# Kernel tuning notes

Hardware: AMD Instinct MI355X
Metric: run time of the kernel (lower is better)

The kernel has to match this reference:

```python
import jax, jax.numpy as jnp
import numpy as np

TEMPERATURE = 0.5

def setup_inputs() -> dict:
    key = jax.random.key(0)
    k1, k2 = jax.random.split(key)
    N, D = 4096, 256
    z1 = jax.random.normal(k1, (N, D), dtype=jnp.float32)
    z2 = jax.random.normal(k2, (N, D), dtype=jnp.float32)
    return {"z1": z1, "z2": z2}

def reference(z1, z2):
    N, D = z1.shape
    # Interleave rows: Z[::2] = z1, Z[1::2] = z2  -> shape (2N, D)
    Z = jnp.stack([z1, z2], axis=1).reshape(2 * N, D).astype(jnp.float32)
    # L2 normalize rows (torch F.normalize default eps=1e-12)
    Z = Z / jnp.maximum(jnp.linalg.norm(Z, axis=1, keepdims=True), 1e-12)
    # Dense exp-similarity matrix (2N, 2N)
    S = jnp.exp(jnp.matmul(Z, Z.T) / TEMPERATURE)
    idx = jnp.arange(2 * N)
    diag = jnp.diagonal(S)
    rowsum = jnp.sum(S, axis=1)
    # positive pair of row i is row i^1 (2i <-> 2i+1)
    pos = S[idx, idx ^ 1]
    loss_per_row = -jnp.log(pos / (rowsum - diag + 1e-8))
    return jnp.sum(loss_per_row) / (2 * N)
```

## Files before the change

### kernel.cpp

```cpp
#include <hip/hip_runtime.h>
#include <hip/hip_bf16.h>
#include <stdint.h>

#define N2 8192
#define D 256
#define DB 512
#define RB_ROWS 256
#define WAVE_ROWS 64
#define CHUNK 32
#define JSPLIT 16
#define COLS_PER_BLOCK (N2 / JSPLIT)
#define CHUNKS_PER_BLOCK (COLS_PER_BLOCK / CHUNK)

using short8 = __attribute__((ext_vector_type(8))) short;
using f32x4  = __attribute__((ext_vector_type(4))) float;

__device__ inline unsigned short f2bf(float x) {
    union { float f; uint32_t u; } a; a.f = x;
    uint32_t r = (a.u + 0x7fff + ((a.u >> 16) & 1)) >> 16;
    return (unsigned short)r;
}

__global__ void knorm(const float* __restrict__ z1, const float* __restrict__ z2,
                      unsigned short* __restrict__ Zb, float* __restrict__ den) {
    int tid  = threadIdx.x;
    int lane = tid & 63;
    int w    = tid >> 6;
    int row  = blockIdx.x * 4 + w;
    const float* src = (row & 1) ? z2 : z1;
    int srow = row >> 1;
    float4 v = reinterpret_cast<const float4*>(src + (size_t)srow * D)[lane];
    float ss = v.x*v.x + v.y*v.y + v.z*v.z + v.w*v.w;
    #pragma unroll
    for (int off = 1; off < 64; off <<= 1) ss += __shfl_xor(ss, off);
    float inv = rsqrtf(ss);
    ushort4 o;
    o.x = f2bf(v.x * inv); o.y = f2bf(v.y * inv);
    o.z = f2bf(v.z * inv); o.w = f2bf(v.w * inv);
    *reinterpret_cast<ushort4*>(Zb + (size_t)row * D + lane * 4) = o;

    int gid = blockIdx.x * blockDim.x + tid;
    if (gid < N2) den[gid] = 0.f;
}

__launch_bounds__(256, 2)
__global__ void kmain(const unsigned short* __restrict__ Zb,
                      float* __restrict__ den, float* __restrict__ pos) {
    __shared__ char tile[CHUNK * DB];
    int tid  = threadIdx.x;
    int lane = tid & 63;
    int w    = tid >> 6;
    int bid  = blockIdx.x;
    int rb   = bid & 31;
    int js   = bid >> 5;
    int Rw   = rb * RB_ROWS + w * WAVE_ROWS;
    int Cbase = js * COLS_PER_BLOCK;
    int l15 = lane & 15, g = lane >> 4;

    const char* Zc = reinterpret_cast<const char*>(Zb);

    short8 A[4][8];
    #pragma unroll
    for (int mf = 0; mf < 4; ++mf) {
        const char* rowp = Zc + (size_t)(Rw + mf*16 + l15) * DB + g*16;
        #pragma unroll
        for (int s = 0; s < 8; ++s)
            A[mf][s] = *reinterpret_cast<const short8*>(rowp + s*64);
    }

    f32x4 acc[4][2];
    float rsum[4][4];
    #pragma unroll
    for (int mf = 0; mf < 4; ++mf) {
        #pragma unroll
        for (int r = 0; r < 4; ++r) rsum[mf][r] = 0.f;
        #pragma unroll
        for (int nf = 0; nf < 2; ++nf) acc[mf][nf] = (f32x4){0.f,0.f,0.f,0.f};
    }

    for (int c = 0; c < CHUNKS_PER_BLOCK; ++c) {
        int C0 = Cbase + c * CHUNK;
        __syncthreads();
        #pragma unroll
        for (int i = 0; i < 4; ++i) {
            int q  = tid + 256 * i;
            int r  = q >> 5;
            int cb = (q & 31) * 16;
            uint4 v = *reinterpret_cast<const uint4*>(Zc + (size_t)(C0 + r) * DB + cb);
            *reinterpret_cast<uint4*>(&tile[r * DB + (cb ^ ((r & 7) << 4))]) = v;
        }
        __syncthreads();

        #pragma unroll
        for (int s = 0; s < 8; ++s) {
            int cb = s*64 + g*16;
            int r0 = l15, r1 = 16 + l15;
            short8 B0 = *reinterpret_cast<const short8*>(&tile[r0 * DB + (cb ^ ((r0 & 7) << 4))]);
            short8 B1 = *reinterpret_cast<const short8*>(&tile[r1 * DB + (cb ^ ((r1 & 7) << 4))]);
            #pragma unroll
            for (int mf = 0; mf < 4; ++mf) {
                acc[mf][0] = __builtin_amdgcn_mfma_f32_16x16x32_bf16(A[mf][s], B0, acc[mf][0], 0, 0, 0);
                acc[mf][1] = __builtin_amdgcn_mfma_f32_16x16x32_bf16(A[mf][s], B1, acc[mf][1], 0, 0, 0);
            }
        }

        #pragma unroll
        for (int mf = 0; mf < 4; ++mf) {
            int Rt = Rw + mf * 16;
            #pragma unroll
            for (int nf = 0; nf < 2; ++nf) {
                int Ct = C0 + nf * 16;
                bool dg = (Ct == Rt);
                #pragma unroll
                for (int r = 0; r < 4; ++r) {
                    float v = acc[mf][nf][r];
                    float e = __expf(v + v);
                    if (dg) {
                        int rl = g * 4 + r;
                        if (l15 == rl) e = 0.f;
                        if (l15 == (rl ^ 1)) pos[Rt + rl] = v;
                    }
                    rsum[mf][r] += e;
                    acc[mf][nf][r] = 0.f;
                }
            }
        }
    }

    #pragma unroll
    for (int mf = 0; mf < 4; ++mf) {
        #pragma unroll
        for (int r = 0; r < 4; ++r) {
            float v = rsum[mf][r];
            v += __shfl_xor(v, 1); v += __shfl_xor(v, 2);
            v += __shfl_xor(v, 4); v += __shfl_xor(v, 8);
            if (l15 == 0) atomicAdd(&den[Rw + mf*16 + g*4 + r], v);
        }
    }
}

__global__ void kloss(const float* __restrict__ den, const float* __restrict__ pos,
                      float* __restrict__ out) {
    __shared__ float red[4];
    int t = threadIdx.x;
    float s = 0.f;
    for (int i = t; i < N2; i += 256)
        s += logf(den[i] + 1e-8f) - 2.f * pos[i];
    #pragma unroll
    for (int off = 1; off < 64; off <<= 1) s += __shfl_xor(s, off);
    if ((t & 63) == 0) red[t >> 6] = s;
    __syncthreads();
    if (t == 0) out[0] = (red[0] + red[1] + red[2] + red[3]) * (1.f / (float)N2);
}

extern "C" void kernel_launch(void* const* d_in, const int* in_sizes, int n_in,
                              void* d_out, int out_size, void* d_ws, size_t ws_size,
                              hipStream_t stream) {
    const float* z1 = (const float*)d_in[0];
    const float* z2 = (const float*)d_in[1];
    char* ws = (char*)d_ws;
    unsigned short* Zb = (unsigned short*)ws;
    float* den = (float*)(ws + (size_t)N2 * DB);
    float* pos = (float*)(ws + (size_t)N2 * DB + (size_t)N2 * 4);

    knorm<<<N2 / 4, 256, 0, stream>>>(z1, z2, Zb, den);
    kmain<<<32 * JSPLIT, 256, 0, stream>>>(Zb, den, pos);
    kloss<<<1, 256, 0, stream>>>(den, pos, (float*)d_out);
}
```

Baseline: 111.7 us.

## Double-buffer column tiles via async global-to-LDS loads and widen blocks to 512 threads

Column tiles are now staged with global_load_lds straight into a double-buffered shared array, so the next chunk's load overlaps the current chunk's MFMA work. Blocks grow to 8 waves of 32 rows each, which halves per-wave register footprint and aims for higher occupancy. The exp is rewritten as exp2 with a folded constant, and the final loss reduction is spread over 32 blocks with an atomic add plus an output memset. The risks are the hand-written vmcnt waits and the extra barrier per chunk, and each B tile from shared memory is now reused by fewer MFMAs.

```diff
diff --git a/kernel.cpp b/kernel.cpp
--- a/kernel.cpp
+++ b/kernel.cpp
@@ -6,14 +6,18 @@
 #define D 256
 #define DB 512
 #define RB_ROWS 256
-#define WAVE_ROWS 64
+#define WAVE_ROWS 32
 #define CHUNK 32
 #define JSPLIT 16
 #define COLS_PER_BLOCK (N2 / JSPLIT)
 #define CHUNKS_PER_BLOCK (COLS_PER_BLOCK / CHUNK)
+#define SWZ(r, b) ((b) ^ (((r) & 7) << 4))
 
 using short8 = __attribute__((ext_vector_type(8))) short;
 using f32x4  = __attribute__((ext_vector_type(4))) float;
+
+typedef __attribute__((address_space(1))) const char gchar_t;
+typedef __attribute__((address_space(3))) char       lchar_t;
 
 __device__ inline unsigned short f2bf(float x) {
     union { float f; uint32_t u; } a; a.f = x;
@@ -43,10 +47,10 @@
     if (gid < N2) den[gid] = 0.f;
 }
 
-__launch_bounds__(256, 2)
+__launch_bounds__(512, 4)
 __global__ void kmain(const unsigned short* __restrict__ Zb,
                       float* __restrict__ den, float* __restrict__ pos) {
-    __shared__ char tile[CHUNK * DB];
+    __shared__ char tile[2][CHUNK * DB];
     int tid  = threadIdx.x;
     int lane = tid & 63;
     int w    = tid >> 6;
@@ -59,53 +63,74 @@
 
     const char* Zc = reinterpret_cast<const char*>(Zb);
 
-    short8 A[4][8];
+    short8 A[2][8];
     #pragma unroll
-    for (int mf = 0; mf < 4; ++mf) {
+    for (int mf = 0; mf < 2; ++mf) {
         const char* rowp = Zc + (size_t)(Rw + mf*16 + l15) * DB + g*16;
         #pragma unroll
         for (int s = 0; s < 8; ++s)
             A[mf][s] = *reinterpret_cast<const short8*>(rowp + s*64);
     }
 
-    f32x4 acc[4][2];
-    float rsum[4][4];
+    int soff[2];
     #pragma unroll
-    for (int mf = 0; mf < 4; ++mf) {
+    for (int k = 0; k < 2; ++k) {
+        int r = w*4 + k*2 + (lane >> 5);
+        int y = (lane & 31) * 16;
+        soff[k] = r * DB + SWZ(r, y);
+    }
+
+    float rsum[2][4];
+    #pragma unroll
+    for (int mf = 0; mf < 2; ++mf)
         #pragma unroll
         for (int r = 0; r < 4; ++r) rsum[mf][r] = 0.f;
-        #pragma unroll
-        for (int nf = 0; nf < 2; ++nf) acc[mf][nf] = (f32x4){0.f,0.f,0.f,0.f};
-    }
+
+    const size_t cb0 = (size_t)Cbase * DB;
+
+    #define STAGE(bf, coff)                                                          \
+        __builtin_amdgcn_global_load_lds(                                            \
+            (gchar_t*)(Zc + (coff) + soff[0]),                                       \
+            (lchar_t*)(&tile[bf][(w*4 + 0) * DB]), 16, 0, 0);                        \
+        __builtin_amdgcn_global_load_lds(                                            \
+            (gchar_t*)(Zc + (coff) + soff[1]),                                       \
+            (lchar_t*)(&tile[bf][(w*4 + 2) * DB]), 16, 0, 0);
+
+    STAGE(0, cb0);
+    int buf = 0;
 
     for (int c = 0; c < CHUNKS_PER_BLOCK; ++c) {
-        int C0 = Cbase + c * CHUNK;
-        __syncthreads();
+        if (c + 1 < CHUNKS_PER_BLOCK) {
+            STAGE(buf ^ 1, cb0 + (size_t)(c + 1) * CHUNK * DB);
+            asm volatile("s_waitcnt vmcnt(2)" ::: "memory");
+        } else {
+            asm volatile("s_waitcnt vmcnt(0)" ::: "memory");
+        }
+        __builtin_amdgcn_s_barrier();
+        __builtin_amdgcn_sched_barrier(0);
+
+        f32x4 acc[2][2];
         #pragma unroll
-        for (int i = 0; i < 4; ++i) {
-            int q  = tid + 256 * i;
-            int r  = q >> 5;
-            int cb = (q & 31) * 16;
-            uint4 v = *reinterpret_cast<const uint4*>(Zc + (size_t)(C0 + r) * DB + cb);
-            *reinterpret_cast<uint4*>(&tile[r * DB + (cb ^ ((r & 7) << 4))]) = v;
-        }
-        __syncthreads();
+        for (int mf = 0; mf < 2; ++mf)
+            #pragma unroll
+            for (int nf = 0; nf < 2; ++nf) acc[mf][nf] = (f32x4){0.f,0.f,0.f,0.f};
 
         #pragma unroll
         for (int s = 0; s < 8; ++s) {
             int cb = s*64 + g*16;
             int r0 = l15, r1 = 16 + l15;
-            short8 B0 = *reinterpret_cast<const short8*>(&tile[r0 * DB + (cb ^ ((r0 & 7) << 4))]);
-            short8 B1 = *reinterpret_cast<const short8*>(&tile[r1 * DB + (cb ^ ((r1 & 7) << 4))]);
+            short8 B0 = *reinterpret_cast<const short8*>(&tile[buf][r0 * DB + SWZ(r0, cb)]);
+            short8 B1 = *reinterpret_cast<const short8*>(&tile[buf][r1 * DB + SWZ(r1, cb)]);
             #pragma unroll
-            for (int mf = 0; mf < 4; ++mf) {
+            for (int mf = 0; mf < 2; ++mf) {
                 acc[mf][0] = __builtin_amdgcn_mfma_f32_16x16x32_bf16(A[mf][s], B0, acc[mf][0], 0, 0, 0);
                 acc[mf][1] = __builtin_amdgcn_mfma_f32_16x16x32_bf16(A[mf][s], B1, acc[mf][1], 0, 0, 0);
             }
         }
 
+        int C0 = Cbase + c * CHUNK;
         #pragma unroll
-        for (int mf = 0; mf < 4; ++mf) {
+        for (int mf = 0; mf < 2; ++mf) {
             int Rt = Rw + mf * 16;
             #pragma unroll
             for (int nf = 0; nf < 2; ++nf) {
@@ -114,21 +139,23 @@
                 #pragma unroll
                 for (int r = 0; r < 4; ++r) {
                     float v = acc[mf][nf][r];
-                    float e = __expf(v + v);
+                    float e = exp2f(v * 2.885390081777927f);
                     if (dg) {
                         int rl = g * 4 + r;
                         if (l15 == rl) e = 0.f;
                         if (l15 == (rl ^ 1)) pos[Rt + rl] = v;
                     }
                     rsum[mf][r] += e;
-                    acc[mf][nf][r] = 0.f;
                 }
             }
         }
+        __builtin_amdgcn_sched_barrier(0);
+        __builtin_amdgcn_s_barrier();
+        buf ^= 1;
     }
 
     #pragma unroll
-    for (int mf = 0; mf < 4; ++mf) {
+    for (int mf = 0; mf < 2; ++mf) {
         #pragma unroll
         for (int r = 0; r < 4; ++r) {
             float v = rsum[mf][r];
@@ -142,15 +169,15 @@
 __global__ void kloss(const float* __restrict__ den, const float* __restrict__ pos,
                       float* __restrict__ out) {
     __shared__ float red[4];
-    int t = threadIdx.x;
-    float s = 0.f;
-    for (int i = t; i < N2; i += 256)
-        s += logf(den[i] + 1e-8f) - 2.f * pos[i];
+    int tid = threadIdx.x;
+    int idx = blockIdx.x * 256 + tid;
+    float s = logf(den[idx] + 1e-8f) - 2.f * pos[idx];
     #pragma unroll
     for (int off = 1; off < 64; off <<= 1) s += __shfl_xor(s, off);
-    if ((t & 63) == 0) red[t >> 6] = s;
+    if ((tid & 63) == 0) red[tid >> 6] = s;
     __syncthreads();
-    if (t == 0) out[0] = (red[0] + red[1] + red[2] + red[3]) * (1.f / (float)N2);
+    if (tid == 0)
+        atomicAdd(out, (red[0] + red[1] + red[2] + red[3]) * (1.f / (float)N2));
 }
 
 extern "C" void kernel_launch(void* const* d_in, const int* in_sizes, int n_in,
@@ -163,7 +190,8 @@
     float* den = (float*)(ws + (size_t)N2 * DB);
     float* pos = (float*)(ws + (size_t)N2 * DB + (size_t)N2 * 4);
 
+    hipMemsetAsync(d_out, 0, sizeof(float), stream);
     knorm<<<N2 / 4, 256, 0, stream>>>(z1, z2, Zb, den);
-    kmain<<<32 * JSPLIT, 256, 0, stream>>>(Zb, den, pos);
-    kloss<<<1, 256, 0, stream>>>(den, pos, (float*)d_out);
+    kmain<<<32 * JSPLIT, 512, 0, stream>>>(Zb, den, pos);
+    kloss<<<N2 / 256, 256, 0, stream>>>(den, pos, (float*)d_out);
 }
```

After: 104.5 us. 1.07x faster.
